# Performance work log

Hardware: AMD Instinct MI355X
Metric: run time of the kernel (lower is better)

## Reference

```python
import jax, jax.numpy as jnp
import numpy as np

# dims: batch, seq, model dim, heads, head_k_dim, head_v_dim, conv size
B, S, D, H, DK, DV, K = 1, 2048, 1024, 8, 128, 128, 4
KD, VD = H * DK, H * DV  # key_dim, value_dim


def _silu(x):
    return x * jax.nn.sigmoid(x)


def _l2norm(x, eps=1e-6):
    return x * jax.lax.rsqrt(jnp.sum(x * x, -1, keepdims=True) + eps)


def _causal_conv_silu(x, w):
    # depthwise causal conv1d (ShortConvolution, activation='silu', no bias)
    # x: [b, s, d], w: [d, K]
    Kc = w.shape[1]
    xp = jnp.pad(x, ((0, 0), (Kc - 1, 0), (0, 0)))
    y = sum(xp[:, i:i + x.shape[1], :] * w[:, i] for i in range(Kc))
    return _silu(y)


def _rmsnorm(x, w, eps=1e-5):
    return x * jax.lax.rsqrt(jnp.mean(x * x, -1, keepdims=True) + eps) * w


def _kda(q, k, v, g, beta):
    # gated delta-rule linear attention (KDA), recurrent form == chunk_kda math
    # q,k,g: [B,S,H,DK]; v: [B,S,H,DV]; beta: [B,S,H]
    scale = DK ** -0.5
    qn = _l2norm(q) * scale  # use_qk_l2norm_in_kernel=True
    kn = _l2norm(k)

    def step(Sm, inp):
        q_t, k_t, v_t, g_t, b_t = inp  # [B,H,DK], [B,H,DK], [B,H,DV], [B,H,DK], [B,H]
        Sm = Sm * jnp.exp(g_t)[..., None]                    # per-key-channel decay
        v_new = (v_t - jnp.einsum('bhk,bhkv->bhv', k_t, Sm)) * b_t[..., None]
        Sm = Sm + k_t[..., None] * v_new[..., None, :]       # delta-rule update
        o_t = jnp.einsum('bhk,bhkv->bhv', q_t, Sm)
        return Sm, o_t

    xs = (jnp.swapaxes(qn, 0, 1), jnp.swapaxes(kn, 0, 1), jnp.swapaxes(v, 0, 1),
          jnp.swapaxes(g, 0, 1), jnp.swapaxes(beta, 0, 1))
    S0 = jnp.zeros((q.shape[0], H, DK, DV), jnp.float32)
    _, o = jax.lax.scan(step, S0, xs)
    return jnp.swapaxes(o, 0, 1)  # [B,S,H,DV]


def setup_inputs() -> dict:
    key = jax.random.key(0)
    ks = jax.random.split(key, 20)

    def w(k, shape, fan_in):
        return jax.random.normal(k, shape, jnp.float32) / np.sqrt(fan_in)

    return {
        'x': jax.random.normal(ks[0], (B, S, D), jnp.float32),
        've': jax.random.normal(ks[1], (B, S, D), jnp.float32),
        'sa_lambdas': jax.random.uniform(ks[2], (2,), jnp.float32),
        'Wq': w(ks[3], (KD, D), D), 'Wk': w(ks[4], (KD, D), D), 'Wv': w(ks[5], (VD, D), D),
        'Wo': w(ks[6], (D, VD), VD),
        'wq_conv': w(ks[7], (KD, K), K), 'wk_conv': w(ks[8], (KD, K), K), 'wv_conv': w(ks[9], (VD, K), K),
        'Wf1': w(ks[10], (DV, D), D), 'Wf2': w(ks[11], (KD, DV), DV),
        'Wb': w(ks[12], (H, D), D),
        'A_log': jnp.log(jax.random.uniform(ks[13], (H,), jnp.float32, 1.0, 16.0)),
        'dt_bias': jnp.zeros((KD,), jnp.float32),
        'Wg1': w(ks[14], (DV, D), D), 'Wg2': w(ks[15], (VD, DV), DV),
        'bg2': jnp.zeros((VD,), jnp.float32),
        'w_norm': jnp.ones((DV,), jnp.float32),
    }


def reference(x, ve, sa_lambdas, Wq, Wk, Wv, Wo, wq_conv, wk_conv, wv_conv,
              Wf1, Wf2, Wb, A_log, dt_bias, Wg1, Wg2, bg2, w_norm):
    b, s, _ = x.shape
    # q/k/v projections + short causal conv with silu
    q = _causal_conv_silu(x @ Wq.T, wq_conv)
    k = _causal_conv_silu(x @ Wk.T, wk_conv)
    v = _causal_conv_silu(x @ Wv.T, wv_conv)
    # fused_kda_gate: g = -exp(A_log) * softplus(f_proj(x) + dt_bias), per [H, DK]
    g = (x @ Wf1.T) @ Wf2.T
    g = jax.nn.softplus((g + dt_bias).astype(jnp.float32)).reshape(b, s, H, DK)
    g = -jnp.exp(A_log)[None, None, :, None] * g
    beta = jax.nn.sigmoid((x @ Wb.T).astype(jnp.float32))  # [b,s,H]
    q = q.reshape(b, s, H, DK)
    k = k.reshape(b, s, H, DK)
    v = v.reshape(b, s, H, DV)
    # mix v with value-embedding ve (3-D branch of _mix_v_with_ve)
    ve_v = _causal_conv_silu(ve @ Wv.T, wv_conv).reshape(b, s, H, DV)
    v = sa_lambdas[0] * v + sa_lambdas[1] * ve_v
    o = _kda(q, k, v, g, beta)  # [b,s,H,DV]
    # FusedRMSNormGated(activation='sigmoid'): rmsnorm(o)*w then gate
    g_out = ((x @ Wg1.T) @ Wg2.T + bg2).reshape(b, s, H, DV)
    o = _rmsnorm(o, w_norm) * jax.nn.sigmoid(g_out)
    return o.reshape(b, s, VD) @ Wo.T
```

## Files before the change

### kernel.cpp

```cpp
#include <hip/hip_runtime.h>
#include <math.h>
#include <stdint.h>

#define S_LEN 2048
#define DMODEL 1024
#define NH 8
#define DK_ 128
#define DV_ 128
#define KD_ 1024
#define KCONV 4
#define CW 32
#define NW2 64
#define PREB_STRIDE 17408
#define TKH_OFF 0
#define QHT_OFF 4096
#define KCT_OFF 8192
#define TV_OFF 12288
#define NN_OFF 16384
#define RS 164
#define GS 20

typedef short bf16x8 __attribute__((ext_vector_type(8)));
typedef float f32x4 __attribute__((ext_vector_type(4)));

__device__ __forceinline__ uint16_t f2bf(float f) {
  uint32_t u = __float_as_uint(f);
  u += 0x7FFF + ((u >> 16) & 1);
  return (uint16_t)(u >> 16);
}
__device__ __forceinline__ float bf2f(uint16_t u) {
  return __uint_as_float((uint32_t)u << 16);
}
__device__ __forceinline__ void glds16(const uint16_t* g, uint16_t* l) {
  __builtin_amdgcn_global_load_lds(
      (const __attribute__((address_space(1))) void*)g,
      (__attribute__((address_space(3))) void*)l, 16, 0, 0);
}
__device__ __forceinline__ float dot4(float4 a, float4 b) {
  return fmaf(a.w, b.w, fmaf(a.z, b.z, fmaf(a.y, b.y, a.x * b.x)));
}
__device__ __forceinline__ float4 f4add(float4 a, float4 b) {
  float4 r; r.x = a.x + b.x; r.y = a.y + b.y; r.z = a.z + b.z; r.w = a.w + b.w; return r;
}
__device__ __forceinline__ float4 f4sub(float4 a, float4 b) {
  float4 r; r.x = a.x - b.x; r.y = a.y - b.y; r.z = a.z - b.z; r.w = a.w - b.w; return r;
}
__device__ __forceinline__ float4 f4mul(float4 a, float4 b) {
  float4 r; r.x = a.x * b.x; r.y = a.y * b.y; r.z = a.z * b.z; r.w = a.w * b.w; return r;
}
__device__ __forceinline__ float4 f4s(float4 a, float s) {
  float4 r; r.x = a.x * s; r.y = a.y * s; r.z = a.z * s; r.w = a.w * s; return r;
}
__device__ __forceinline__ float4 f4expc(float4 a) {
  float4 r;
  r.x = expf(fminf(a.x, 0.f)); r.y = expf(fminf(a.y, 0.f));
  r.z = expf(fminf(a.z, 0.f)); r.w = expf(fminf(a.w, 0.f));
  return r;
}
__device__ __forceinline__ float4 f4exp(float4 a) {
  float4 r; r.x = expf(a.x); r.y = expf(a.y); r.z = expf(a.z); r.w = expf(a.w); return r;
}
__device__ __forceinline__ uint4 pack8(float4 a, float4 b) {
  uint4 r;
  r.x = (uint32_t)f2bf(a.x) | ((uint32_t)f2bf(a.y) << 16);
  r.y = (uint32_t)f2bf(a.z) | ((uint32_t)f2bf(a.w) << 16);
  r.z = (uint32_t)f2bf(b.x) | ((uint32_t)f2bf(b.y) << 16);
  r.w = (uint32_t)f2bf(b.z) | ((uint32_t)f2bf(b.w) << 16);
  return r;
}
__device__ __forceinline__ uint2 pack4(f32x4 a) {
  uint2 r;
  r.x = (uint32_t)f2bf(a[0]) | ((uint32_t)f2bf(a[1]) << 16);
  r.y = (uint32_t)f2bf(a[2]) | ((uint32_t)f2bf(a[3]) << 16);
  return r;
}
union U4B8 { uint4 u; bf16x8 b; };
__device__ __forceinline__ bf16x8 u2b(uint4 u) { U4B8 x; x.u = u; return x.b; }

#define DPPADD(x, ctrl) \
  x += __int_as_float(__builtin_amdgcn_update_dpp(0, __float_as_int(x), ctrl, 0xF, 0xF, true))

__device__ __forceinline__ void row8_sum2(float& a, float& b) {
  DPPADD(a, 0xB1); DPPADD(b, 0xB1);
  DPPADD(a, 0x4E); DPPADD(b, 0x4E);
  DPPADD(a, 0x141); DPPADD(b, 0x141);
}
__device__ __forceinline__ void row8_arr8x2(float* x, float* y) {
#pragma unroll
  for (int i = 0; i < 8; i++) { DPPADD(x[i], 0xB1); DPPADD(y[i], 0xB1); }
#pragma unroll
  for (int i = 0; i < 8; i++) { DPPADD(x[i], 0x4E); DPPADD(y[i], 0x4E); }
#pragma unroll
  for (int i = 0; i < 8; i++) { DPPADD(x[i], 0x141); DPPADD(y[i], 0x141); }
}

struct CastArgs {
  const float* s[8];
  uint16_t* d[8];
  int n[8];
};
__global__ __launch_bounds__(256) void cast_multi(CastArgs a) {
  int i = blockIdx.y;
  const int step = gridDim.x * 256 * 8;
  for (int base = (blockIdx.x * 256 + threadIdx.x) * 8; base < a.n[i]; base += step) {
    const float4* sp = (const float4*)(a.s[i] + base);
    float4 x0 = sp[0], x1 = sp[1];
    *(uint4*)(a.d[i] + base) = pack8(x0, x1);
  }
}

__global__ __launch_bounds__(256) void gemm_wc(
    const float* __restrict__ A,
    const float* __restrict__ B,
    uint16_t* __restrict__ C) {
  __shared__ float As[16][68];
  __shared__ float Bs[16][68];
  const int tid = threadIdx.x;
  const int m0 = blockIdx.y * 64, n0 = blockIdx.x * 64;
  const int tx = tid & 15, ty = tid >> 4;
  const int lk = tid & 15, lr = tid >> 4;
  const int bc = tid & 63, bkr = tid >> 6;
  float acc[4][4] = {};
  for (int k0 = 0; k0 < 128; k0 += 16) {
#pragma unroll
    for (int i = 0; i < 4; i++) {
      As[lk][lr + 16 * i] = A[(size_t)(m0 + lr + 16 * i) * 128 + k0 + lk];
      Bs[bkr + 4 * i][bc] = B[(size_t)(k0 + bkr + 4 * i) * 1024 + n0 + bc];
    }
    __syncthreads();
#pragma unroll
    for (int kk = 0; kk < 16; kk++) {
      float4 a4 = *(const float4*)&As[kk][ty * 4];
      float4 b4 = *(const float4*)&Bs[kk][tx * 4];
      float av[4] = {a4.x, a4.y, a4.z, a4.w};
      float bv[4] = {b4.x, b4.y, b4.z, b4.w};
#pragma unroll
      for (int i = 0; i < 4; i++)
#pragma unroll
        for (int jx = 0; jx < 4; jx++) acc[i][jx] = fmaf(av[i], bv[jx], acc[i][jx]);
    }
    __syncthreads();
  }
#pragma unroll
  for (int i = 0; i < 4; i++)
#pragma unroll
    for (int jx = 0; jx < 4; jx++)
      C[(size_t)(m0 + ty * 4 + i) * 1024 + n0 + tx * 4 + jx] = f2bf(acc[i][jx]);
}

__global__ __launch_bounds__(256) void pad_wb(const float* __restrict__ Wb,
                                              uint16_t* __restrict__ Wbp) {
  int idx = blockIdx.x * 256 + threadIdx.x;
  if (idx >= 128 * 1024) return;
  int r = idx >> 10;
  Wbp[idx] = (r < 8) ? f2bf(Wb[idx]) : (uint16_t)0;
}

struct GJobs {
  const uint16_t* A[8];
  const uint16_t* B[8];
  void* C[8];
  int N[8];
  int outbf[8];
};
__global__ __launch_bounds__(256) void gemm_mfma(GJobs j, int K) {
  const int z = blockIdx.z;
  const int N = j.N[z];
  const int n0 = blockIdx.x * 128;
  if (n0 >= N) return;
  __shared__ uint16_t Asb[128 * 32];
  __shared__ uint16_t Bsb[128 * 32];
  const uint16_t* __restrict__ A = j.A[z];
  const uint16_t* __restrict__ B = j.B[z];
  const int tid = threadIdx.x;
  const int w = tid >> 6, lane = tid & 63;
  const int m0 = blockIdx.y * 128;
  const int mw = (w & 1) * 64, nw = (w >> 1) * 64;
  const int c0 = tid, c1 = 256 + tid;
  const int r0 = c0 >> 2, cl0 = (c0 & 3) ^ ((r0 >> 2) & 3);
  const int r1 = c1 >> 2, cl1 = (c1 & 3) ^ ((r1 >> 2) & 3);
  const uint16_t* gA0 = A + (size_t)(m0 + r0) * K + cl0 * 8;
  const uint16_t* gA1 = A + (size_t)(m0 + r1) * K + cl1 * 8;
  const uint16_t* gB0 = B + (size_t)(n0 + r0) * K + cl0 * 8;
  const uint16_t* gB1 = B + (size_t)(n0 + r1) * K + cl1 * 8;
  uint16_t* lA0 = Asb + w * 512;
  uint16_t* lA1 = Asb + 2048 + w * 512;
  uint16_t* lB0 = Bsb + w * 512;
  uint16_t* lB1 = Bsb + 2048 + w * 512;

  const int l15 = lane & 15, q = lane >> 4;
  const int ccq = q ^ ((l15 >> 2) & 3);

  f32x4 acc[4][4] = {};
  for (int k0 = 0; k0 < K; k0 += 32) {
    glds16(gA0 + k0, lA0);
    glds16(gA1 + k0, lA1);
    glds16(gB0 + k0, lB0);
    glds16(gB1 + k0, lB1);
    __syncthreads();
    bf16x8 af[4], bfr[4];
#pragma unroll
    for (int i = 0; i < 4; i++)
      af[i] = *(const bf16x8*)&Asb[(mw + i * 16 + l15) * 32 + ccq * 8];
#pragma unroll
    for (int jx = 0; jx < 4; jx++)
      bfr[jx] = *(const bf16x8*)&Bsb[(nw + jx * 16 + l15) * 32 + ccq * 8];
#pragma unroll
    for (int i = 0; i < 4; i++)
#pragma unroll
      for (int jx = 0; jx < 4; jx++)
        acc[i][jx] = __builtin_amdgcn_mfma_f32_16x16x32_bf16(af[i], bfr[jx],
                                                             acc[i][jx], 0, 0, 0);
    __syncthreads();
  }
  const int obf = j.outbf[z];
#pragma unroll
  for (int i = 0; i < 4; i++) {
#pragma unroll
    for (int jx = 0; jx < 4; jx++) {
      int n = n0 + nw + jx * 16 + l15;
#pragma unroll
      for (int r = 0; r < 4; r++) {
        int m = m0 + mw + i * 16 + q * 4 + r;
        if (obf)
          ((uint16_t*)j.C[z])[(size_t)m * N + n] = f2bf(acc[i][jx][r]);
        else
          ((float*)j.C[z])[(size_t)m * N + n] = acc[i][jx][r];
      }
    }
  }
}

__global__ __launch_bounds__(256) void conv_silu_mix(
    const uint16_t* __restrict__ qp, const uint16_t* __restrict__ kp,
    const uint16_t* __restrict__ vp, const uint16_t* __restrict__ vep,
    const float* __restrict__ wq, const float* __restrict__ wk,
    const float* __restrict__ wv, const float* __restrict__ lam,
    float* __restrict__ qc, float* __restrict__ kc, float* __restrict__ vmx) {
  int idx = blockIdx.x * 256 + threadIdx.x;
  if (idx >= S_LEN * KD_) return;
  int s = idx >> 10, d = idx & 1023;
  float aq = 0.f, ak = 0.f, av = 0.f, ae = 0.f;
#pragma unroll
  for (int i = 0; i < KCONV; i++) {
    int ss = s - (KCONV - 1) + i;
    if (ss < 0) continue;
    size_t off = (size_t)ss * KD_ + d;
    aq = fmaf(bf2f(qp[off]), wq[d * KCONV + i], aq);
    ak = fmaf(bf2f(kp[off]), wk[d * KCONV + i], ak);
    av = fmaf(bf2f(vp[off]), wv[d * KCONV + i], av);
    ae = fmaf(bf2f(vep[off]), wv[d * KCONV + i], ae);
  }
  qc[idx] = aq / (1.f + expf(-aq));
  kc[idx] = ak / (1.f + expf(-ak));
  float sv = av / (1.f + expf(-av));
  float se = ae / (1.f + expf(-ae));
  vmx[idx] = lam[0] * sv + lam[1] * se;
}

__global__ __launch_bounds__(256) void kda_pre(
    const float* __restrict__ qc, const float* __restrict__ kc,
    const float* __restrict__ graw, const float* __restrict__ vm,
    const float* __restrict__ bpre, const float* __restrict__ dt_bias,
    const float* __restrict__ A_log, uint16_t* __restrict__ preB,
    float* __restrict__ preF) {
  __shared__ float kls[32 * RS];
  __shared__ float Gls[32 * RS];
  __shared__ float Mcm[32 * 36];
  __shared__ float bls[32];
  const int w = blockIdx.x >> 3, h = blockIdx.x & 7;
  const int tid = threadIdx.x;
  const int t = tid >> 3, kq = tid & 7;
  const int wv = tid >> 6;
  const size_t gb = (size_t)blockIdx.x * PREB_STRIDE;
  const size_t gf = (size_t)blockIdx.x * 128;

  size_t roff = (size_t)(w * CW + t) * KD_ + h * DK_ + kq * 16;
  float4 kv[4], qv[4], gv[4], dtb[4];
#pragma unroll
  for (int i = 0; i < 4; i++) {
    kv[i] = *(const float4*)(kc + roff + i * 4);
    qv[i] = *(const float4*)(qc + roff + i * 4);
    gv[i] = *(const float4*)(graw + roff + i * 4);
    dtb[i] = *(const float4*)(dt_bias + h * DK_ + kq * 16 + i * 4);
  }
  const float Ahead = expf(A_log[h]);
  if (tid < 32) {
    float b = bpre[(size_t)(w * CW + tid) * 128 + h];
    bls[tid] = 1.f / (1.f + expf(-b));
  }
  float src[32];
  if (tid >= 128) {
    int c2 = tid - 128;
#pragma unroll
    for (int t2 = 0; t2 < 32; t2++)
      src[t2] = vm[(size_t)(w * CW + t2) * KD_ + h * DV_ + c2];
  }
#pragma unroll
  for (int i = 0; i < 4; i++) {
    float vsp[4];
    float xin[4] = {gv[i].x + dtb[i].x, gv[i].y + dtb[i].y,
                    gv[i].z + dtb[i].z, gv[i].w + dtb[i].w};
#pragma unroll
    for (int e = 0; e < 4; e++)
      vsp[e] = (xin[e] > 20.f) ? xin[e] : log1pf(expf(xin[e]));
    gv[i].x = -Ahead * vsp[0]; gv[i].y = -Ahead * vsp[1];
    gv[i].z = -Ahead * vsp[2]; gv[i].w = -Ahead * vsp[3];
  }
  float sk = 0.f, sq = 0.f;
#pragma unroll
  for (int i = 0; i < 4; i++) {
    sk += dot4(kv[i], kv[i]);
    sq += dot4(qv[i], qv[i]);
  }
  row8_sum2(sk, sq);
  float rkn = rsqrtf(sk + 1e-6f);
  float rqn = rsqrtf(sq + 1e-6f) * 0.08838834764831845f;
#pragma unroll
  for (int i = 0; i < 4; i++) {
    kv[i] = f4s(kv[i], rkn);
    qv[i] = f4s(qv[i], rqn);
    *(float4*)&kls[t * RS + kq * GS + i * 4] = kv[i];
    *(float4*)&Gls[t * RS + kq * GS + i * 4] = gv[i];
  }
  __syncthreads();
  float4 Ga[4] = {};
#pragma unroll
  for (int jb = 0; jb < 4; jb++) {
    if (jb <= wv) {
#pragma unroll
      for (int jj = 0; jj < 8; jj++) {
        int j = jb * 8 + jj;
        bool inc = (jb < wv) || (j <= t);
#pragma unroll
        for (int i = 0; i < 4; i++) {
          float4 gj = *(const float4*)&Gls[j * RS + kq * GS + i * 4];
          if (inc) Ga[i] = f4add(Ga[i], gj);
        }
      }
    }
  }
  __syncthreads();
  float4 khr[4];
  float4 Pa[4];
#pragma unroll
  for (int i = 0; i < 4; i++) {
    *(float4*)&Gls[t * RS + kq * GS + i * 4] = Ga[i];
    Pa[i] = f4exp(Ga[i]);
    khr[i] = f4mul(kv[i], Pa[i]);
  }
  {
    float4 q0 = f4mul(qv[0], Pa[0]), q1 = f4mul(qv[1], Pa[1]);
    float4 q2 = f4mul(qv[2], Pa[2]), q3 = f4mul(qv[3], Pa[3]);
    *(uint4*)(preB + gb + QHT_OFF + t * 128 + kq * 16) = pack8(q0, q1);
    *(uint4*)(preB + gb + QHT_OFF + t * 128 + kq * 16 + 8) = pack8(q2, q3);
  }
  if (t == 31) {
#pragma unroll
    for (int i = 0; i < 4; i++)
      *(float4*)(preF + gf + kq * 16 + i * 4) = Pa[i];
  }
  __syncthreads();
#pragma unroll
  for (int i = 0; i < 4; i++) {
    float4 Gfi = *(const float4*)&Gls[31 * RS + kq * GS + i * 4];
    float4 ea = f4expc(f4sub(Gfi, Ga[i]));
    float4 kc4 = f4mul(kv[i], ea);
    float kk[4] = {kc4.x, kc4.y, kc4.z, kc4.w};
#pragma unroll
    for (int e = 0; e < 4; e++)
      preB[gb + KCT_OFF + (kq * 16 + i * 4 + e) * 32 + t] = f2bf(kk[e]);
  }
#pragma unroll
  for (int jb = 0; jb < 4; jb++) {
    if (jb <= wv) {
      float mp8[8], np8[8];
#pragma unroll
      for (int jj = 0; jj < 8; jj++) {
        int j = jb * 8 + jj;
        float m = 0.f, n = 0.f;
#pragma unroll
        for (int i = 0; i < 4; i++) {
          float4 kj = *(const float4*)&kls[j * RS + kq * GS + i * 4];
          float4 Gj = *(const float4*)&Gls[j * RS + kq * GS + i * 4];
          float4 e = f4expc(f4sub(Ga[i], Gj));
          float4 p = f4mul(kj, e);
          m += dot4(kv[i], p);
          n += dot4(qv[i], p);
        }
        mp8[jj] = (j < t) ? m : 0.f;
        np8[jj] = (j <= t) ? n : 0.f;
      }
      row8_arr8x2(mp8, np8);
#pragma unroll
      for (int jj = 0; jj < 8; jj++) {
        if (kq == jj) {
          int j = jb * 8 + jj;
          Mcm[j * 36 + t] = bls[t] * mp8[jj];
          preB[gb + NN_OFF + t * 32 + j] = f2bf(np8[jj]);
        }
      }
    } else {
      preB[gb + NN_OFF + t * 32 + jb * 8 + kq] = 0;
    }
  }
  float bl[32];
#pragma unroll
  for (int i = 0; i < 8; i++) {
    float4 b4 = *(const float4*)&bls[i * 4];
    bl[i * 4 + 0] = b4.x; bl[i * 4 + 1] = b4.y;
    bl[i * 4 + 2] = b4.z; bl[i * 4 + 3] = b4.w;
  }
  __syncthreads();
#pragma unroll
  for (int i = 0; i < 4; i++)
    *(float4*)&kls[t * RS + kq * GS + i * 4] = khr[i];
  __syncthreads();
  if (tid < 128) {
#pragma unroll
    for (int t2 = 0; t2 < 32; t2++)
      src[t2] = kls[t2 * RS + (tid >> 4) * GS + (tid & 15)];
  }
  const int c = tid;
  float acc[32];
#pragma unroll
  for (int i = 0; i < 32; i++) acc[i] = 0.f;
#pragma unroll
  for (int t2 = 0; t2 < 32; t2++) {
    float val = fmaf(bl[t2], src[t2], -acc[t2]);
    if (c < 128)
      preB[gb + TKH_OFF + t2 * 128 + c] = f2bf(val);
    else
      preB[gb + TV_OFF + t2 * 128 + (c - 128)] = f2bf(val);
#pragma unroll
    for (int t3 = t2 + 1; t3 < 32; t3++)
      acc[t3] = fmaf(Mcm[t2 * 36 + t3], val, acc[t3]);
  }
}

__global__ __launch_bounds__(128) void kda_scan(
    const uint16_t* __restrict__ preB, const float* __restrict__ preF,
    float* __restrict__ o) {
  __shared__ uint16_t tkh[2][32 * 136];
  __shared__ uint16_t qht[2][32 * 136];
  __shared__ uint16_t sbf[16 * 136];
  __shared__ uint16_t vbf[16 * 40];
  const int h = blockIdx.x & 7, cg = blockIdx.x >> 3;
  const int tid = threadIdx.x;
  const int wv = tid >> 6, lane = tid & 63;
  const int q = lane >> 4, l15 = lane & 15;

  auto stage = [&](int w, int buf) {
    size_t gbs = (size_t)(w * 8 + h) * PREB_STRIDE;
    const uint4* gt = (const uint4*)(preB + gbs + TKH_OFF);
    const uint4* gq = (const uint4*)(preB + gbs + QHT_OFF);
    int row = lane >> 1, half = lane & 1;
    uint4 a[8], b[8];
#pragma unroll
    for (int i = 0; i < 8; i++) {
      a[i] = gt[lane * 8 + i];
      b[i] = gq[lane * 8 + i];
    }
#pragma unroll
    for (int i = 0; i < 8; i++) {
      *(uint4*)&tkh[buf][row * 136 + half * 64 + i * 8] = a[i];
      *(uint4*)&qht[buf][row * 136 + half * 64 + i * 8] = b[i];
    }
  };

  f32x4 s[8] = {};

  if (wv == 1) stage(0, 0);
  __syncthreads();

  for (int w = 0; w < NW2; w++) {
    if (wv == 1) {
      if (w + 1 < NW2) stage(w + 1, (w + 1) & 1);
    } else {
      const int buf = w & 1;
      const size_t gbs = (size_t)(w * 8 + h) * PREB_STRIDE;
      uint4 kct[8], nrg[2];
      float4 pb[8];
      float tvv[2][4];
#pragma unroll
      for (int ki = 0; ki < 8; ki++)
        kct[ki] = *(const uint4*)(preB + gbs + KCT_OFF + (16 * ki + l15) * 32 + q * 8);
#pragma unroll
      for (int tt = 0; tt < 2; tt++)
        nrg[tt] = *(const uint4*)(preB + gbs + NN_OFF + (tt * 16 + l15) * 32 + q * 8);
#pragma unroll
      for (int ki = 0; ki < 8; ki++)
        pb[ki] = *(const float4*)(preF + (size_t)(w * 8 + h) * 128 + 16 * ki + q * 4);
#pragma unroll
      for (int tt = 0; tt < 2; tt++)
#pragma unroll
        for (int r = 0; r < 4; r++)
          tvv[tt][r] = bf2f(preB[gbs + TV_OFF + (tt * 16 + q * 4 + r) * 128 + cg * 16 + l15]);
#pragma unroll
      for (int ki = 0; ki < 8; ki++)
        *(uint2*)&sbf[l15 * 136 + 16 * ki + q * 4] = pack4(s[ki]);
      f32x4 aat[2] = {}, bbt[2] = {};
#pragma unroll
      for (int kc = 0; kc < 4; kc++) {
        bf16x8 bS = *(const bf16x8*)&sbf[l15 * 136 + kc * 32 + q * 8];
#pragma unroll
        for (int tt = 0; tt < 2; tt++) {
          bf16x8 aT = *(const bf16x8*)&tkh[buf][(tt * 16 + l15) * 136 + kc * 32 + q * 8];
          bf16x8 aQ = *(const bf16x8*)&qht[buf][(tt * 16 + l15) * 136 + kc * 32 + q * 8];
          aat[tt] = __builtin_amdgcn_mfma_f32_16x16x32_bf16(aT, bS, aat[tt], 0, 0, 0);
          bbt[tt] = __builtin_amdgcn_mfma_f32_16x16x32_bf16(aQ, bS, bbt[tt], 0, 0, 0);
        }
      }
#pragma unroll
      for (int tt = 0; tt < 2; tt++) {
        f32x4 vn;
#pragma unroll
        for (int r = 0; r < 4; r++) vn[r] = tvv[tt][r] - aat[tt][r];
        *(uint2*)&vbf[l15 * 40 + tt * 16 + q * 4] = pack4(vn);
      }
      bf16x8 bV = *(const bf16x8*)&vbf[l15 * 40 + q * 8];
#pragma unroll
      for (int tt = 0; tt < 2; tt++) {
        f32x4 ot = __builtin_amdgcn_mfma_f32_16x16x32_bf16(u2b(nrg[tt]), bV,
                                                           bbt[tt], 0, 0, 0);
#pragma unroll
        for (int r = 0; r < 4; r++)
          o[(size_t)(w * CW + tt * 16 + q * 4 + r) * KD_ + h * DK_ + cg * 16 + l15] = ot[r];
      }
#pragma unroll
      for (int ki = 0; ki < 8; ki++) {
#pragma unroll
        for (int r = 0; r < 4; r++) s[ki][r] *= pb[ki][r];
        s[ki] = __builtin_amdgcn_mfma_f32_16x16x32_bf16(u2b(kct[ki]), bV, s[ki], 0, 0, 0);
      }
    }
    __syncthreads();
  }
}

__global__ __launch_bounds__(64) void gated_rmsnorm(
    const float* __restrict__ o, const float* __restrict__ g2raw,
    const float* __restrict__ bg2, const float* __restrict__ wn,
    uint16_t* __restrict__ ob) {
  size_t base = (size_t)blockIdx.x * DV_;
  int t = threadIdx.x;
  float a = o[base + t], b = o[base + t + 64];
  float ss = a * a + b * b;
#pragma unroll
  for (int off = 32; off > 0; off >>= 1) ss += __shfl_xor(ss, off);
  float r = rsqrtf(ss * (1.f / 128.f) + 1e-5f);
  int c0 = (int)((base + t) & 1023), c1 = (int)((base + t + 64) & 1023);
  float ga = 1.f / (1.f + expf(-(g2raw[base + t] + bg2[c0])));
  float gb = 1.f / (1.f + expf(-(g2raw[base + t + 64] + bg2[c1])));
  ob[base + t] = f2bf(a * r * wn[t] * ga);
  ob[base + t + 64] = f2bf(b * r * wn[t + 64] * gb);
}

extern "C" void kernel_launch(void* const* d_in, const int* in_sizes, int n_in,
                              void* d_out, int out_size, void* d_ws, size_t ws_size,
                              hipStream_t stream) {
  const float* x = (const float*)d_in[0];
  const float* ve = (const float*)d_in[1];
  const float* lam = (const float*)d_in[2];
  const float* Wq = (const float*)d_in[3];
  const float* Wk = (const float*)d_in[4];
  const float* Wv = (const float*)d_in[5];
  const float* Wo = (const float*)d_in[6];
  const float* wq_conv = (const float*)d_in[7];
  const float* wk_conv = (const float*)d_in[8];
  const float* wv_conv = (const float*)d_in[9];
  const float* Wf1 = (const float*)d_in[10];
  const float* Wf2 = (const float*)d_in[11];
  const float* Wb = (const float*)d_in[12];
  const float* A_log = (const float*)d_in[13];
  const float* dt_bias = (const float*)d_in[14];
  const float* Wg1 = (const float*)d_in[15];
  const float* Wg2 = (const float*)d_in[16];
  const float* bg2 = (const float*)d_in[17];
  const float* w_norm = (const float*)d_in[18];
  float* out = (float*)d_out;

  float* ws = (float*)d_ws;
  const size_t SZ = (size_t)S_LEN * KD_;
  uint16_t* qpb = (uint16_t*)ws;
  uint16_t* kpb = (uint16_t*)(ws + SZ / 2);
  uint16_t* vpb = (uint16_t*)(ws + SZ);
  uint16_t* vepb = (uint16_t*)(ws + 3 * SZ / 2);
  float* q_c = ws + 2 * SZ;
  float* k_c = ws + 3 * SZ;
  float* v_mix = ws + 4 * SZ;
  float* graw = ws + 5 * SZ;
  float* o_buf = graw;
  float* g2raw = k_c;
  uint16_t* bws = (uint16_t*)(ws + 6 * SZ);
  uint16_t* xb = bws;
  uint16_t* veb = xb + SZ;
  uint16_t* Wqb = veb + SZ;
  uint16_t* Wkb = Wqb + (size_t)KD_ * DMODEL;
  uint16_t* Wvb = Wkb + (size_t)KD_ * DMODEL;
  uint16_t* Wob = Wvb + (size_t)KD_ * DMODEL;
  uint16_t* Wg1b = Wob + (size_t)DMODEL * KD_;
  uint16_t* Wg2b = Wg1b + (size_t)DV_ * DMODEL;
  uint16_t* Wcb = Wg2b + (size_t)KD_ * DV_;
  uint16_t* Wbp = Wcb + (size_t)KD_ * DMODEL;
  uint16_t* g1b = Wbp + (size_t)128 * 1024;
  uint16_t* ob = g1b + (size_t)S_LEN * DV_;
  float* bpre2 = ws + 18 * (size_t)1024 * 1024;
  float* preF = ws + (size_t)20 * 1024 * 1024;
  uint16_t* preB = (uint16_t*)(ws + (size_t)20 * 1024 * 1024 + 65536 + 64);

  dim3 blk(256);
  int ew_blocks = (S_LEN * KD_ + 255) / 256;

  CastArgs ca;
  ca.s[0] = x;   ca.d[0] = xb;   ca.n[0] = S_LEN * DMODEL;
  ca.s[1] = ve;  ca.d[1] = veb;  ca.n[1] = S_LEN * DMODEL;
  ca.s[2] = Wq;  ca.d[2] = Wqb;  ca.n[2] = KD_ * DMODEL;
  ca.s[3] = Wk;  ca.d[3] = Wkb;  ca.n[3] = KD_ * DMODEL;
  ca.s[4] = Wv;  ca.d[4] = Wvb;  ca.n[4] = KD_ * DMODEL;
  ca.s[5] = Wo;  ca.d[5] = Wob;  ca.n[5] = DMODEL * KD_;
  ca.s[6] = Wg1; ca.d[6] = Wg1b; ca.n[6] = DV_ * DMODEL;
  ca.s[7] = Wg2; ca.d[7] = Wg2b; ca.n[7] = KD_ * DV_;
  cast_multi<<<dim3(256, 8), blk, 0, stream>>>(ca);

  gemm_wc<<<dim3(16, 16), blk, 0, stream>>>(Wf2, Wf1, Wcb);
  pad_wb<<<dim3(512), blk, 0, stream>>>(Wb, Wbp);

  GJobs jq;
  jq.A[0] = xb;  jq.B[0] = Wqb;  jq.C[0] = qpb;   jq.N[0] = KD_; jq.outbf[0] = 1;
  jq.A[1] = xb;  jq.B[1] = Wkb;  jq.C[1] = kpb;   jq.N[1] = KD_; jq.outbf[1] = 1;
  jq.A[2] = xb;  jq.B[2] = Wvb;  jq.C[2] = vpb;   jq.N[2] = KD_; jq.outbf[2] = 1;
  jq.A[3] = veb; jq.B[3] = Wvb;  jq.C[3] = vepb;  jq.N[3] = KD_; jq.outbf[3] = 1;
  jq.A[4] = xb;  jq.B[4] = Wg1b; jq.C[4] = g1b;   jq.N[4] = DV_; jq.outbf[4] = 1;
  jq.A[5] = xb;  jq.B[5] = Wcb;  jq.C[5] = graw;  jq.N[5] = KD_; jq.outbf[5] = 0;
  jq.A[6] = xb;  jq.B[6] = Wbp;  jq.C[6] = bpre2; jq.N[6] = 128; jq.outbf[6] = 0;
  gemm_mfma<<<dim3(8, 16, 7), blk, 0, stream>>>(jq, DMODEL);

  conv_silu_mix<<<ew_blocks, blk, 0, stream>>>(qpb, kpb, vpb, vepb,
                                               wq_conv, wk_conv, wv_conv, lam,
                                               q_c, k_c, v_mix);

  kda_pre<<<dim3(NW2 * 8), blk, 0, stream>>>(q_c, k_c, graw, v_mix, bpre2,
                                             dt_bias, A_log, preB, preF);
  kda_scan<<<dim3(64), dim3(128), 0, stream>>>(preB, preF, o_buf);

  GJobs jg2;
  jg2.A[0] = g1b; jg2.B[0] = Wg2b; jg2.C[0] = g2raw; jg2.N[0] = KD_; jg2.outbf[0] = 0;
  gemm_mfma<<<dim3(8, 16, 1), blk, 0, stream>>>(jg2, DV_);

  gated_rmsnorm<<<dim3(S_LEN * NH), dim3(64), 0, stream>>>(o_buf, g2raw, bg2,
                                                           w_norm, ob);

  GJobs jo;
  jo.A[0] = ob; jo.B[0] = Wob; jo.C[0] = out; jo.N[0] = DMODEL; jo.outbf[0] = 0;
  gemm_mfma<<<dim3(8, 16, 1), blk, 0, stream>>>(jo, KD_);
}
```

Baseline: 392.2 us.

## Replace producer-wave LDS staging in scan with register double-buffered prefetch

The KDA scan kernel drops its second producer wave and the double-buffered shared-memory staging of the T/Q operand tiles. A single wave now loads every per-chunk operand (T, Q, kct, nrg, decay, tv) straight from global memory into registers, with two register sets alternating so chunk w+2 is fetched while chunk w is computed. This removes the per-chunk __syncthreads and the LDS round trip for the A operands on the serial critical path. The cost is much higher register pressure, which risks spills, and the loads must now hide their latency within a single wave's instruction stream.

```diff
diff --git a/kernel.cpp b/kernel.cpp
--- a/kernel.cpp
+++ b/kernel.cpp
@@ -438,103 +438,97 @@
   }
 }
 
-__global__ __launch_bounds__(128) void kda_scan(
+__global__ __launch_bounds__(64) void kda_scan(
     const uint16_t* __restrict__ preB, const float* __restrict__ preF,
     float* __restrict__ o) {
-  __shared__ uint16_t tkh[2][32 * 136];
-  __shared__ uint16_t qht[2][32 * 136];
   __shared__ uint16_t sbf[16 * 136];
   __shared__ uint16_t vbf[16 * 40];
   const int h = blockIdx.x & 7, cg = blockIdx.x >> 3;
   const int tid = threadIdx.x;
-  const int wv = tid >> 6, lane = tid & 63;
-  const int q = lane >> 4, l15 = lane & 15;
-
-  auto stage = [&](int w, int buf) {
-    size_t gbs = (size_t)(w * 8 + h) * PREB_STRIDE;
-    const uint4* gt = (const uint4*)(preB + gbs + TKH_OFF);
-    const uint4* gq = (const uint4*)(preB + gbs + QHT_OFF);
-    int row = lane >> 1, half = lane & 1;
-    uint4 a[8], b[8];
-#pragma unroll
-    for (int i = 0; i < 8; i++) {
-      a[i] = gt[lane * 8 + i];
-      b[i] = gq[lane * 8 + i];
-    }
-#pragma unroll
-    for (int i = 0; i < 8; i++) {
-      *(uint4*)&tkh[buf][row * 136 + half * 64 + i * 8] = a[i];
-      *(uint4*)&qht[buf][row * 136 + half * 64 + i * 8] = b[i];
-    }
+  const int q = tid >> 4, l15 = tid & 15;
+
+  f32x4 s[8] = {};
+
+  auto pload = [&](uint4 (&aT)[8], uint4 (&aQ)[8], uint4 (&kct)[8],
+                   uint4 (&nrg)[2], float4 (&pb)[8], float (&tvv)[8], int w) {
+    const size_t gbs = (size_t)(w * 8 + h) * PREB_STRIDE;
+#pragma unroll
+    for (int tt = 0; tt < 2; tt++)
+#pragma unroll
+      for (int kc = 0; kc < 4; kc++) {
+        aT[tt * 4 + kc] = *(const uint4*)(preB + gbs + TKH_OFF +
+                                          (tt * 16 + l15) * 128 + kc * 32 + q * 8);
+        aQ[tt * 4 + kc] = *(const uint4*)(preB + gbs + QHT_OFF +
+                                          (tt * 16 + l15) * 128 + kc * 32 + q * 8);
+      }
+#pragma unroll
+    for (int ki = 0; ki < 8; ki++)
+      kct[ki] = *(const uint4*)(preB + gbs + KCT_OFF + (16 * ki + l15) * 32 + q * 8);
+#pragma unroll
+    for (int tt = 0; tt < 2; tt++)
+      nrg[tt] = *(const uint4*)(preB + gbs + NN_OFF + (tt * 16 + l15) * 32 + q * 8);
+#pragma unroll
+    for (int ki = 0; ki < 8; ki++)
+      pb[ki] = *(const float4*)(preF + (size_t)(w * 8 + h) * 128 + 16 * ki + q * 4);
+#pragma unroll
+    for (int tt = 0; tt < 2; tt++)
+#pragma unroll
+      for (int r = 0; r < 4; r++)
+        tvv[tt * 4 + r] =
+            bf2f(preB[gbs + TV_OFF + (tt * 16 + q * 4 + r) * 128 + cg * 16 + l15]);
   };
 
-  f32x4 s[8] = {};
-
-  if (wv == 1) stage(0, 0);
-  __syncthreads();
-
-  for (int w = 0; w < NW2; w++) {
-    if (wv == 1) {
-      if (w + 1 < NW2) stage(w + 1, (w + 1) & 1);
-    } else {
-      const int buf = w & 1;
-      const size_t gbs = (size_t)(w * 8 + h) * PREB_STRIDE;
-      uint4 kct[8], nrg[2];
-      float4 pb[8];
-      float tvv[2][4];
-#pragma unroll
-      for (int ki = 0; ki < 8; ki++)
-        kct[ki] = *(const uint4*)(preB + gbs + KCT_OFF + (16 * ki + l15) * 32 + q * 8);
-#pragma unroll
-      for (int tt = 0; tt < 2; tt++)
-        nrg[tt] = *(const uint4*)(preB + gbs + NN_OFF + (tt * 16 + l15) * 32 + q * 8);
-#pragma unroll
-      for (int ki = 0; ki < 8; ki++)
-        pb[ki] = *(const float4*)(preF + (size_t)(w * 8 + h) * 128 + 16 * ki + q * 4);
-#pragma unroll
-      for (int tt = 0; tt < 2; tt++)
-#pragma unroll
-        for (int r = 0; r < 4; r++)
-          tvv[tt][r] = bf2f(preB[gbs + TV_OFF + (tt * 16 + q * 4 + r) * 128 + cg * 16 + l15]);
-#pragma unroll
-      for (int ki = 0; ki < 8; ki++)
-        *(uint2*)&sbf[l15 * 136 + 16 * ki + q * 4] = pack4(s[ki]);
-      f32x4 aat[2] = {}, bbt[2] = {};
-#pragma unroll
-      for (int kc = 0; kc < 4; kc++) {
-        bf16x8 bS = *(const bf16x8*)&sbf[l15 * 136 + kc * 32 + q * 8];
-#pragma unroll
-        for (int tt = 0; tt < 2; tt++) {
-          bf16x8 aT = *(const bf16x8*)&tkh[buf][(tt * 16 + l15) * 136 + kc * 32 + q * 8];
-          bf16x8 aQ = *(const bf16x8*)&qht[buf][(tt * 16 + l15) * 136 + kc * 32 + q * 8];
-          aat[tt] = __builtin_amdgcn_mfma_f32_16x16x32_bf16(aT, bS, aat[tt], 0, 0, 0);
-          bbt[tt] = __builtin_amdgcn_mfma_f32_16x16x32_bf16(aQ, bS, bbt[tt], 0, 0, 0);
-        }
+  auto compute = [&](uint4 (&aT)[8], uint4 (&aQ)[8], uint4 (&kct)[8],
+                     uint4 (&nrg)[2], float4 (&pb)[8], float (&tvv)[8], int w) {
+#pragma unroll
+    for (int ki = 0; ki < 8; ki++)
+      *(uint2*)&sbf[l15 * 136 + 16 * ki + q * 4] = pack4(s[ki]);
+    f32x4 aat[2] = {}, bbt[2] = {};
+#pragma unroll
+    for (int kc = 0; kc < 4; kc++) {
+      bf16x8 bS = *(const bf16x8*)&sbf[l15 * 136 + kc * 32 + q * 8];
+#pragma unroll
+      for (int tt = 0; tt < 2; tt++) {
+        aat[tt] = __builtin_amdgcn_mfma_f32_16x16x32_bf16(u2b(aT[tt * 4 + kc]), bS,
+                                                          aat[tt], 0, 0, 0);
+        bbt[tt] = __builtin_amdgcn_mfma_f32_16x16x32_bf16(u2b(aQ[tt * 4 + kc]), bS,
+                                                          bbt[tt], 0, 0, 0);
       }
-#pragma unroll
-      for (int tt = 0; tt < 2; tt++) {
-        f32x4 vn;
-#pragma unroll
-        for (int r = 0; r < 4; r++) vn[r] = tvv[tt][r] - aat[tt][r];
-        *(uint2*)&vbf[l15 * 40 + tt * 16 + q * 4] = pack4(vn);
-      }
-      bf16x8 bV = *(const bf16x8*)&vbf[l15 * 40 + q * 8];
-#pragma unroll
-      for (int tt = 0; tt < 2; tt++) {
-        f32x4 ot = __builtin_amdgcn_mfma_f32_16x16x32_bf16(u2b(nrg[tt]), bV,
-                                                           bbt[tt], 0, 0, 0);
-#pragma unroll
-        for (int r = 0; r < 4; r++)
-          o[(size_t)(w * CW + tt * 16 + q * 4 + r) * KD_ + h * DK_ + cg * 16 + l15] = ot[r];
-      }
-#pragma unroll
-      for (int ki = 0; ki < 8; ki++) {
-#pragma unroll
-        for (int r = 0; r < 4; r++) s[ki][r] *= pb[ki][r];
-        s[ki] = __builtin_amdgcn_mfma_f32_16x16x32_bf16(u2b(kct[ki]), bV, s[ki], 0, 0, 0);
-      }
-    }
-    __syncthreads();
+    }
+#pragma unroll
+    for (int tt = 0; tt < 2; tt++) {
+      f32x4 vn;
+#pragma unroll
+      for (int r = 0; r < 4; r++) vn[r] = tvv[tt * 4 + r] - aat[tt][r];
+      *(uint2*)&vbf[l15 * 40 + tt * 16 + q * 4] = pack4(vn);
+    }
+    bf16x8 bV = *(const bf16x8*)&vbf[l15 * 40 + q * 8];
+#pragma unroll
+    for (int tt = 0; tt < 2; tt++) {
+      f32x4 ot = __builtin_amdgcn_mfma_f32_16x16x32_bf16(u2b(nrg[tt]), bV,
+                                                         bbt[tt], 0, 0, 0);
+#pragma unroll
+      for (int r = 0; r < 4; r++)
+        o[(size_t)(w * CW + tt * 16 + q * 4 + r) * KD_ + h * DK_ + cg * 16 + l15] =
+            ot[r];
+    }
+#pragma unroll
+    for (int ki = 0; ki < 8; ki++) {
+#pragma unroll
+      for (int r = 0; r < 4; r++) s[ki][r] *= pb[ki][r];
+      s[ki] = __builtin_amdgcn_mfma_f32_16x16x32_bf16(u2b(kct[ki]), bV, s[ki], 0, 0, 0);
+    }
+  };
+
+  uint4 aTA[8], aQA[8], kcA[8], nrA[2]; float4 pbA[8]; float tvA[8];
+  uint4 aTB[8], aQB[8], kcB[8], nrB[2]; float4 pbB[8]; float tvB[8];
+  pload(aTA, aQA, kcA, nrA, pbA, tvA, 0);
+  pload(aTB, aQB, kcB, nrB, pbB, tvB, 1);
+  for (int w = 0; w < NW2; w += 2) {
+    compute(aTA, aQA, kcA, nrA, pbA, tvA, w);
+    if (w + 2 < NW2) pload(aTA, aQA, kcA, nrA, pbA, tvA, w + 2);
+    compute(aTB, aQB, kcB, nrB, pbB, tvB, w + 1);
+    if (w + 3 < NW2) pload(aTB, aQB, kcB, nrB, pbB, tvB, w + 3);
   }
 }
 
@@ -642,7 +636,7 @@
 
   kda_pre<<<dim3(NW2 * 8), blk, 0, stream>>>(q_c, k_c, graw, v_mix, bpre2,
                                              dt_bias, A_log, preB, preF);
-  kda_scan<<<dim3(64), dim3(128), 0, stream>>>(preB, preF, o_buf);
+  kda_scan<<<dim3(64), dim3(64), 0, stream>>>(preB, preF, o_buf);
 
   GJobs jg2;
   jg2.A[0] = g1b; jg2.B[0] = Wg2b; jg2.C[0] = g2raw; jg2.N[0] = KD_; jg2.outbf[0] = 0;
```

Measured after the change: 420.9 us. +7.3%, slower.

## Co-schedule g2 GEMM with scan kernel, fold Wb padding into cast, vectorize conv

Applied to the files above, without the earlier changes.

Runs the small g1×Wg2 GEMM on extra blocks of the latency-bound scan kernel, so it uses otherwise idle CUs instead of needing its own launch. The Wb pad/cast moves into cast_multi as a ninth grid row, removing another launch. The conv+silu kernel now handles 8 channels per thread with 16-byte loads and stores. The trade-off is that the scan now uses 256-thread blocks with two waves doing nothing, plus extra shared memory for the GEMM tiles, which could hurt scan occupancy or scheduling.

```diff
diff --git a/kernel.cpp b/kernel.cpp
--- a/kernel.cpp
+++ b/kernel.cpp
@@ -99,8 +99,16 @@
   uint16_t* d[8];
   int n[8];
 };
-__global__ __launch_bounds__(256) void cast_multi(CastArgs a) {
+__global__ __launch_bounds__(256) void cast_multi(CastArgs a, const float* __restrict__ Wb,
+                                                  uint16_t* __restrict__ Wbp) {
   int i = blockIdx.y;
+  if (i == 8) {
+    for (int idx = blockIdx.x * 256 + threadIdx.x; idx < 128 * 1024; idx += 256 * 256) {
+      int r = idx >> 10;
+      Wbp[idx] = (r < 8) ? f2bf(Wb[idx]) : (uint16_t)0;
+    }
+    return;
+  }
   const int step = gridDim.x * 256 * 8;
   for (int base = (blockIdx.x * 256 + threadIdx.x) * 8; base < a.n[i]; base += step) {
     const float4* sp = (const float4*)(a.s[i] + base);
@@ -148,33 +156,14 @@
       C[(size_t)(m0 + ty * 4 + i) * 1024 + n0 + tx * 4 + jx] = f2bf(acc[i][jx]);
 }
 
-__global__ __launch_bounds__(256) void pad_wb(const float* __restrict__ Wb,
-                                              uint16_t* __restrict__ Wbp) {
-  int idx = blockIdx.x * 256 + threadIdx.x;
-  if (idx >= 128 * 1024) return;
-  int r = idx >> 10;
-  Wbp[idx] = (r < 8) ? f2bf(Wb[idx]) : (uint16_t)0;
-}
-
-struct GJobs {
-  const uint16_t* A[8];
-  const uint16_t* B[8];
-  void* C[8];
-  int N[8];
-  int outbf[8];
-};
-__global__ __launch_bounds__(256) void gemm_mfma(GJobs j, int K) {
-  const int z = blockIdx.z;
-  const int N = j.N[z];
-  const int n0 = blockIdx.x * 128;
+__device__ __forceinline__ void gemm_body(
+    const uint16_t* __restrict__ A, const uint16_t* __restrict__ B, void* C,
+    int N, int K, int outbf, int bx, int by, int tid,
+    uint16_t* Asb, uint16_t* Bsb) {
+  const int n0 = bx * 128;
   if (n0 >= N) return;
-  __shared__ uint16_t Asb[128 * 32];
-  __shared__ uint16_t Bsb[128 * 32];
-  const uint16_t* __restrict__ A = j.A[z];
-  const uint16_t* __restrict__ B = j.B[z];
-  const int tid = threadIdx.x;
   const int w = tid >> 6, lane = tid & 63;
-  const int m0 = blockIdx.y * 128;
+  const int m0 = by * 128;
   const int mw = (w & 1) * 64, nw = (w >> 1) * 64;
   const int c0 = tid, c1 = 256 + tid;
   const int r0 = c0 >> 2, cl0 = (c0 & 3) ^ ((r0 >> 2) & 3);
@@ -213,7 +202,6 @@
                                                              acc[i][jx], 0, 0, 0);
     __syncthreads();
   }
-  const int obf = j.outbf[z];
 #pragma unroll
   for (int i = 0; i < 4; i++) {
 #pragma unroll
@@ -222,13 +210,28 @@
 #pragma unroll
       for (int r = 0; r < 4; r++) {
         int m = m0 + mw + i * 16 + q * 4 + r;
-        if (obf)
-          ((uint16_t*)j.C[z])[(size_t)m * N + n] = f2bf(acc[i][jx][r]);
+        if (outbf)
+          ((uint16_t*)C)[(size_t)m * N + n] = f2bf(acc[i][jx][r]);
         else
-          ((float*)j.C[z])[(size_t)m * N + n] = acc[i][jx][r];
+          ((float*)C)[(size_t)m * N + n] = acc[i][jx][r];
       }
     }
   }
+}
+
+struct GJobs {
+  const uint16_t* A[8];
+  const uint16_t* B[8];
+  void* C[8];
+  int N[8];
+  int outbf[8];
+};
+__global__ __launch_bounds__(256) void gemm_mfma(GJobs j, int K) {
+  __shared__ uint16_t Asb[128 * 32];
+  __shared__ uint16_t Bsb[128 * 32];
+  const int z = blockIdx.z;
+  gemm_body(j.A[z], j.B[z], j.C[z], j.N[z], K, j.outbf[z],
+            blockIdx.x, blockIdx.y, threadIdx.x, Asb, Bsb);
 }
 
 __global__ __launch_bounds__(256) void conv_silu_mix(
@@ -238,24 +241,86 @@
     const float* __restrict__ wv, const float* __restrict__ lam,
     float* __restrict__ qc, float* __restrict__ kc, float* __restrict__ vmx) {
   int idx = blockIdx.x * 256 + threadIdx.x;
-  if (idx >= S_LEN * KD_) return;
-  int s = idx >> 10, d = idx & 1023;
-  float aq = 0.f, ak = 0.f, av = 0.f, ae = 0.f;
-#pragma unroll
-  for (int i = 0; i < KCONV; i++) {
-    int ss = s - (KCONV - 1) + i;
-    if (ss < 0) continue;
-    size_t off = (size_t)ss * KD_ + d;
-    aq = fmaf(bf2f(qp[off]), wq[d * KCONV + i], aq);
-    ak = fmaf(bf2f(kp[off]), wk[d * KCONV + i], ak);
-    av = fmaf(bf2f(vp[off]), wv[d * KCONV + i], av);
-    ae = fmaf(bf2f(vep[off]), wv[d * KCONV + i], ae);
-  }
-  qc[idx] = aq / (1.f + expf(-aq));
-  kc[idx] = ak / (1.f + expf(-ak));
-  float sv = av / (1.f + expf(-av));
-  float se = ae / (1.f + expf(-ae));
-  vmx[idx] = lam[0] * sv + lam[1] * se;
+  if (idx >= S_LEN * KD_ / 8) return;
+  int s = idx >> 7;
+  int d0 = (idx & 127) * 8;
+  const float lam0 = lam[0], lam1 = lam[1];
+
+  union { uint4 u; ushort h[8]; } t;
+  size_t base = (size_t)s * KD_ + d0;
+
+  {
+    float4 w4[8];
+#pragma unroll
+    for (int c = 0; c < 8; c++) w4[c] = *(const float4*)(wq + (size_t)d0 * 4 + c * 4);
+    float acc[8] = {};
+#pragma unroll
+    for (int i = 0; i < KCONV; i++) {
+      int ss = s - (KCONV - 1) + i;
+      if (ss < 0) continue;
+      t.u = *(const uint4*)(qp + (size_t)ss * KD_ + d0);
+      float wi[8] = {w4[0].x, w4[1].x, w4[2].x, w4[3].x, w4[4].x, w4[5].x, w4[6].x, w4[7].x};
+      if (i == 1) { for (int c = 0; c < 8; c++) wi[c] = ((const float*)&w4[c])[1]; }
+      if (i == 2) { for (int c = 0; c < 8; c++) wi[c] = ((const float*)&w4[c])[2]; }
+      if (i == 3) { for (int c = 0; c < 8; c++) wi[c] = ((const float*)&w4[c])[3]; }
+#pragma unroll
+      for (int c = 0; c < 8; c++) acc[c] = fmaf(bf2f(t.h[c]), wi[c], acc[c]);
+    }
+    float out[8];
+#pragma unroll
+    for (int c = 0; c < 8; c++) out[c] = acc[c] / (1.f + expf(-acc[c]));
+    *(float4*)(qc + base) = *(float4*)&out[0];
+    *(float4*)(qc + base + 4) = *(float4*)&out[4];
+  }
+  {
+    float4 w4[8];
+#pragma unroll
+    for (int c = 0; c < 8; c++) w4[c] = *(const float4*)(wk + (size_t)d0 * 4 + c * 4);
+    float acc[8] = {};
+#pragma unroll
+    for (int i = 0; i < KCONV; i++) {
+      int ss = s - (KCONV - 1) + i;
+      if (ss < 0) continue;
+      t.u = *(const uint4*)(kp + (size_t)ss * KD_ + d0);
+#pragma unroll
+      for (int c = 0; c < 8; c++)
+        acc[c] = fmaf(bf2f(t.h[c]), ((const float*)&w4[c])[i], acc[c]);
+    }
+    float out[8];
+#pragma unroll
+    for (int c = 0; c < 8; c++) out[c] = acc[c] / (1.f + expf(-acc[c]));
+    *(float4*)(kc + base) = *(float4*)&out[0];
+    *(float4*)(kc + base + 4) = *(float4*)&out[4];
+  }
+  {
+    float4 w4[8];
+#pragma unroll
+    for (int c = 0; c < 8; c++) w4[c] = *(const float4*)(wv + (size_t)d0 * 4 + c * 4);
+    float av[8] = {}, ae[8] = {};
+#pragma unroll
+    for (int i = 0; i < KCONV; i++) {
+      int ss = s - (KCONV - 1) + i;
+      if (ss < 0) continue;
+      size_t off = (size_t)ss * KD_ + d0;
+      t.u = *(const uint4*)(vp + off);
+#pragma unroll
+      for (int c = 0; c < 8; c++)
+        av[c] = fmaf(bf2f(t.h[c]), ((const float*)&w4[c])[i], av[c]);
+      t.u = *(const uint4*)(vep + off);
+#pragma unroll
+      for (int c = 0; c < 8; c++)
+        ae[c] = fmaf(bf2f(t.h[c]), ((const float*)&w4[c])[i], ae[c]);
+    }
+    float out[8];
+#pragma unroll
+    for (int c = 0; c < 8; c++) {
+      float sv = av[c] / (1.f + expf(-av[c]));
+      float se = ae[c] / (1.f + expf(-ae[c]));
+      out[c] = lam0 * sv + lam1 * se;
+    }
+    *(float4*)(vmx + base) = *(float4*)&out[0];
+    *(float4*)(vmx + base + 4) = *(float4*)&out[4];
+  }
 }
 
 __global__ __launch_bounds__(256) void kda_pre(
@@ -438,15 +503,26 @@
   }
 }
 
-__global__ __launch_bounds__(128) void kda_scan(
+__global__ __launch_bounds__(256) void kda_scan_g2(
     const uint16_t* __restrict__ preB, const float* __restrict__ preF,
-    float* __restrict__ o) {
+    float* __restrict__ o, const uint16_t* __restrict__ g1b,
+    const uint16_t* __restrict__ Wg2b, float* __restrict__ g2raw) {
   __shared__ uint16_t tkh[2][32 * 136];
   __shared__ uint16_t qht[2][32 * 136];
   __shared__ uint16_t sbf[16 * 136];
   __shared__ uint16_t vbf[16 * 40];
-  const int h = blockIdx.x & 7, cg = blockIdx.x >> 3;
+  __shared__ uint16_t Asb[128 * 32];
+  __shared__ uint16_t Bsb[128 * 32];
+  const int bid = blockIdx.x;
   const int tid = threadIdx.x;
+
+  if (bid >= 64) {
+    int b2 = bid - 64;
+    gemm_body(g1b, Wg2b, g2raw, 1024, 128, 0, b2 & 7, b2 >> 3, tid, Asb, Bsb);
+    return;
+  }
+
+  const int h = bid & 7, cg = bid >> 3;
   const int wv = tid >> 6, lane = tid & 63;
   const int q = lane >> 4, l15 = lane & 15;
 
@@ -476,7 +552,7 @@
   for (int w = 0; w < NW2; w++) {
     if (wv == 1) {
       if (w + 1 < NW2) stage(w + 1, (w + 1) & 1);
-    } else {
+    } else if (wv == 0) {
       const int buf = w & 1;
       const size_t gbs = (size_t)(w * 8 + h) * PREB_STRIDE;
       uint4 kct[8], nrg[2];
@@ -610,7 +686,6 @@
   uint16_t* preB = (uint16_t*)(ws + (size_t)20 * 1024 * 1024 + 65536 + 64);
 
   dim3 blk(256);
-  int ew_blocks = (S_LEN * KD_ + 255) / 256;
 
   CastArgs ca;
   ca.s[0] = x;   ca.d[0] = xb;   ca.n[0] = S_LEN * DMODEL;
@@ -621,10 +696,9 @@
   ca.s[5] = Wo;  ca.d[5] = Wob;  ca.n[5] = DMODEL * KD_;
   ca.s[6] = Wg1; ca.d[6] = Wg1b; ca.n[6] = DV_ * DMODEL;
   ca.s[7] = Wg2; ca.d[7] = Wg2b; ca.n[7] = KD_ * DV_;
-  cast_multi<<<dim3(256, 8), blk, 0, stream>>>(ca);
+  cast_multi<<<dim3(256, 9), blk, 0, stream>>>(ca, Wb, Wbp);
 
   gemm_wc<<<dim3(16, 16), blk, 0, stream>>>(Wf2, Wf1, Wcb);
-  pad_wb<<<dim3(512), blk, 0, stream>>>(Wb, Wbp);
 
   GJobs jq;
   jq.A[0] = xb;  jq.B[0] = Wqb;  jq.C[0] = qpb;   jq.N[0] = KD_; jq.outbf[0] = 1;
@@ -636,17 +710,15 @@
   jq.A[6] = xb;  jq.B[6] = Wbp;  jq.C[6] = bpre2; jq.N[6] = 128; jq.outbf[6] = 0;
   gemm_mfma<<<dim3(8, 16, 7), blk, 0, stream>>>(jq, DMODEL);
 
-  conv_silu_mix<<<ew_blocks, blk, 0, stream>>>(qpb, kpb, vpb, vepb,
-                                               wq_conv, wk_conv, wv_conv, lam,
-                                               q_c, k_c, v_mix);
+  int conv_blocks = (S_LEN * KD_ / 8 + 255) / 256;
+  conv_silu_mix<<<conv_blocks, blk, 0, stream>>>(qpb, kpb, vpb, vepb,
+                                                 wq_conv, wk_conv, wv_conv, lam,
+                                                 q_c, k_c, v_mix);
 
   kda_pre<<<dim3(NW2 * 8), blk, 0, stream>>>(q_c, k_c, graw, v_mix, bpre2,
                                              dt_bias, A_log, preB, preF);
-  kda_scan<<<dim3(64), dim3(128), 0, stream>>>(preB, preF, o_buf);
-
-  GJobs jg2;
-  jg2.A[0] = g1b; jg2.B[0] = Wg2b; jg2.C[0] = g2raw; jg2.N[0] = KD_; jg2.outbf[0] = 0;
-  gemm_mfma<<<dim3(8, 16, 1), blk, 0, stream>>>(jg2, DV_);
+
+  kda_scan_g2<<<dim3(192), blk, 0, stream>>>(preB, preF, o_buf, g1b, Wg2b, g2raw);
 
   gated_rmsnorm<<<dim3(S_LEN * NH), dim3(64), 0, stream>>>(o_buf, g2raw, bg2,
                                                            w_norm, ob);
```

After: 384.9 us. Within noise of the previous version (-1.9%).
